# Performance work log

Hardware: AMD Instinct MI355X
Metric: run time of the kernel (lower is better)

Reference implementation:

```python
import jax, jax.numpy as jnp
import numpy as np

N_NODE = 100000
N_EDGE = 500000
IN_DIM = 128
OUT_DIM = 128
ATTN_DIM = 64
N_REL = 200
N_Q = 64


def setup_inputs() -> dict:
    key = jax.random.key(0)
    ks = jax.random.split(key, 24)
    # edge table: columns [r_idx, _, rel, _, tau, sub, obj]
    r_idx = jax.random.randint(ks[0], (N_EDGE,), 0, N_Q, dtype=jnp.int32)
    rel = jax.random.randint(ks[1], (N_EDGE,), 0, 2 * N_REL + 1, dtype=jnp.int32)
    tau = jax.random.randint(ks[2], (N_EDGE,), -1, 366, dtype=jnp.int32)  # -1 -> q_tau fallback
    sub = jax.random.randint(ks[3], (N_EDGE,), 0, N_NODE, dtype=jnp.int32)
    obj = jax.random.randint(ks[4], (N_EDGE,), 0, N_NODE, dtype=jnp.int32)
    zeros = jnp.zeros((N_EDGE,), jnp.int32)
    edges = jnp.stack([r_idx, zeros, rel, zeros, tau, sub, obj], axis=1)

    def lin(k, fan_in, fan_out):
        return jax.random.normal(k, (fan_in, fan_out), jnp.float32) * (1.0 / np.sqrt(fan_in))

    return {
        "q_sub": jax.random.randint(ks[5], (N_Q,), 0, N_NODE, dtype=jnp.int32),
        "q_rel": jax.random.randint(ks[6], (N_Q,), 0, 2 * N_REL + 1, dtype=jnp.int32),
        "q_tau": 180,
        "hidden": jax.random.normal(ks[7], (N_NODE, IN_DIM), jnp.float32),
        "edges": edges,
        "n_node": N_NODE,
        "old_nodes_new_idx": jax.random.randint(ks[8], (1000,), 0, N_NODE, dtype=jnp.int32),
        "rela_embed": jax.random.normal(ks[9], (2 * N_REL + 1, IN_DIM), jnp.float32),
        "Ws_w": lin(ks[10], IN_DIM, ATTN_DIM),
        "Wr_w": lin(ks[11], IN_DIM, ATTN_DIM),
        "Wqr_w": lin(ks[12], IN_DIM, ATTN_DIM),
        "Wqr_b": jnp.zeros((ATTN_DIM,), jnp.float32),
        "Wtau_w": lin(ks[13], IN_DIM, ATTN_DIM),
        "w_alpha_w": lin(ks[14], ATTN_DIM, 1),
        "w_alpha_b": jnp.zeros((1,), jnp.float32),
        "W_h_w": lin(ks[15], IN_DIM, OUT_DIM),
        "W_h_s_w": lin(ks[16], IN_DIM, OUT_DIM),
        "weight_t1": jax.random.normal(ks[17], (1, IN_DIM), jnp.float32),
        "bias_t1": jax.random.normal(ks[18], (1, IN_DIM), jnp.float32),
        "weight_t2": jax.random.normal(ks[19], (1, IN_DIM), jnp.float32),
        "bias_t2": jax.random.normal(ks[20], (1, IN_DIM), jnp.float32),
    }


def reference(q_sub, q_rel, q_tau, hidden, edges, n_node, old_nodes_new_idx,
              rela_embed, Ws_w, Wr_w, Wqr_w, Wqr_b, Wtau_w,
              w_alpha_w, w_alpha_b, W_h_w, W_h_s_w,
              weight_t1, bias_t1, weight_t2, bias_t2):
    sub = edges[:, 5]
    rel = edges[:, 2]
    obj = edges[:, 6]
    tau = edges[:, 4]
    r_idx = edges[:, 0]

    hs = hidden[sub]                       # [E, in_dim] gather
    hr = rela_embed[rel]                   # [E, in_dim]
    h_qr = rela_embed[q_rel][r_idx]        # [E, in_dim]

    tau = jnp.where(tau >= 0, tau, q_tau)
    delta = (tau - q_tau).astype(hidden.dtype)[:, None]  # [E, 1]
    h_tau = weight_t1 * delta + bias_t1 + jnp.sin(weight_t2 * delta + bias_t2)

    message = hs + hr + h_tau              # [E, in_dim]

    attn = jax.nn.relu(hs @ Ws_w + hr @ Wr_w + (h_qr @ Wqr_w + Wqr_b) + h_tau @ Wtau_w)
    alpha = jax.nn.sigmoid(attn @ w_alpha_w + w_alpha_b)  # [E, 1]

    msg = alpha * message
    msg_s = (1.0 - alpha) * message

    agg = jax.ops.segment_sum(msg, obj, num_segments=n_node)      # [n_node, in_dim]
    agg_s = jax.ops.segment_sum(msg_s, obj, num_segments=n_node)

    hidden_new = agg @ W_h_w       # act is identity (default lambda x: x)
    hidden_new_s = agg_s @ W_h_s_w
    return hidden_new, hidden_new_s
```

## Files before the change

### kernel.cpp

```cpp
#include <hip/hip_runtime.h>
#include <math.h>

#define N_NODE   100000
#define N_EDGE   500000
#define IN_DIM   128
#define OUT_DIM  128
#define ATTN_DIM 64
#define N_RELTAB 401
#define N_QRY    64
#define N_TAU    366

#define SCAN_BLK     256
#define N_SCAN_BLKS  ((N_NODE + SCAN_BLK - 1) / SCAN_BLK)

typedef unsigned int  uint;
typedef unsigned short ushort;
typedef __attribute__((ext_vector_type(8))) short bf16x8;
typedef __attribute__((ext_vector_type(4))) float f32x4;

__device__ __forceinline__ float bfl(uint u)  { return __uint_as_float(u << 16); }
__device__ __forceinline__ float bfh(uint u)  { return __uint_as_float(u & 0xFFFF0000u); }
__device__ __forceinline__ uint  f2bfbits(float f) {
    uint u = __float_as_uint(f);
    return (u + 0x7FFFu + ((u >> 16) & 1u)) >> 16;
}
__device__ __forceinline__ uint  pack2(float lo, float hi) {
    return f2bfbits(lo) | (f2bfbits(hi) << 16);
}

__global__ void build_tables(const int* __restrict__ q_rel,
                             const int* __restrict__ q_tau_p,
                             const float* __restrict__ rela_embed,
                             const float* __restrict__ Wr_w,
                             const float* __restrict__ Wqr_w,
                             const float* __restrict__ Wqr_b,
                             const float* __restrict__ Wtau_w,
                             const float* __restrict__ w_t1,
                             const float* __restrict__ b_t1,
                             const float* __restrict__ w_t2,
                             const float* __restrict__ b_t2,
                             const float* __restrict__ W_h_w,
                             const float* __restrict__ W_h_s_w,
                             const float* __restrict__ Ws_w,
                             uint* __restrict__ rel_attn_bf,
                             uint* __restrict__ qr_attn_bf,
                             uint* __restrict__ tau_attn_bf,
                             uint* __restrict__ rel_msg_bf,
                             uint* __restrict__ tau_msg_bf,
                             ushort* __restrict__ wT_bf,
                             ushort* __restrict__ wsT_bf) {
    __shared__ float srow[IN_DIM];
    __shared__ float sattn[ATTN_DIM];
    const int b = blockIdx.x;
    const int t = threadIdx.x;

    if (b < N_TAU) {
        const int q_tau = *q_tau_p;
        const float delta = (float)(b - q_tau);
        float v = w_t1[t] * delta + b_t1[t] + sinf(w_t2[t] * delta + b_t2[t]);
        srow[t] = v;
        __syncthreads();
        if (t < 64) tau_msg_bf[b * 64 + t] = pack2(srow[2 * t], srow[2 * t + 1]);
        if (t < ATTN_DIM) {
            float acc = 0.f;
            #pragma unroll 8
            for (int d = 0; d < IN_DIM; ++d)
                acc += srow[d] * Wtau_w[d * ATTN_DIM + t];
            sattn[t] = acc;
        }
        __syncthreads();
        if (t < 32) tau_attn_bf[b * 32 + t] = pack2(sattn[2 * t], sattn[2 * t + 1]);
    } else if (b < N_TAU + N_RELTAB) {
        const int r = b - N_TAU;
        srow[t] = rela_embed[r * IN_DIM + t];
        __syncthreads();
        if (t < 64) rel_msg_bf[r * 64 + t] = pack2(srow[2 * t], srow[2 * t + 1]);
        if (t < ATTN_DIM) {
            float acc = 0.f;
            #pragma unroll 8
            for (int d = 0; d < IN_DIM; ++d)
                acc += srow[d] * Wr_w[d * ATTN_DIM + t];
            sattn[t] = acc;
        }
        __syncthreads();
        if (t < 32) rel_attn_bf[r * 32 + t] = pack2(sattn[2 * t], sattn[2 * t + 1]);
    } else if (b < N_TAU + N_RELTAB + N_QRY) {
        const int i = b - N_TAU - N_RELTAB;
        const int r = q_rel[i];
        srow[t] = rela_embed[r * IN_DIM + t];
        __syncthreads();
        if (t < ATTN_DIM) {
            float acc = Wqr_b[t];
            #pragma unroll 8
            for (int d = 0; d < IN_DIM; ++d)
                acc += srow[d] * Wqr_w[d * ATTN_DIM + t];
            sattn[t] = acc;
        }
        __syncthreads();
        if (t < 32) qr_attn_bf[i * 32 + t] = pack2(sattn[2 * t], sattn[2 * t + 1]);
    } else {
        const int w = b - (N_TAU + N_RELTAB + N_QRY);
        if (w < 2) {
            const float* Wsrc = w ? W_h_s_w : W_h_w;
            ushort* dst = wT_bf + (size_t)w * 128 * 128;
            for (int k = 0; k < 128; ++k)
                dst[t * 128 + k] = (ushort)f2bfbits(Wsrc[k * 128 + t]);
        } else {
            for (int n = 0; n < 64; ++n)
                wsT_bf[n * 128 + t] = (ushort)f2bfbits(Ws_w[t * ATTN_DIM + n]);
        }
    }
}

__global__ __launch_bounds__(256) void node_attn_mfma(const float* __restrict__ hidden,
                                                      const ushort* __restrict__ wsT_bf,
                                                      uint* __restrict__ hid_bf_u,
                                                      ushort* __restrict__ A_node) {
    const int wave = threadIdx.x >> 6;
    const int lane = threadIdx.x & 63;
    const int m    = lane & 15;
    const int quad = lane >> 4;
    const int row0 = blockIdx.x * 64 + wave * 16;
    const int row  = row0 + m;
    const int rowc = min(row, N_NODE - 1);

    const float* hsrc = hidden + (size_t)rowc * IN_DIM;
    ushort* hdst = (ushort*)hid_bf_u + (size_t)rowc * 128;

    bf16x8 afr[4];
    #pragma unroll
    for (int ks = 0; ks < 4; ++ks) {
        const int k0 = ks * 32 + quad * 8;
        const float4 v0 = *(const float4*)(hsrc + k0);
        const float4 v1 = *(const float4*)(hsrc + k0 + 4);
        union { uint u[4]; bf16x8 v; } cvt;
        cvt.u[0] = pack2(v0.x, v0.y);
        cvt.u[1] = pack2(v0.z, v0.w);
        cvt.u[2] = pack2(v1.x, v1.y);
        cvt.u[3] = pack2(v1.z, v1.w);
        afr[ks] = cvt.v;
        if (row < N_NODE) *(bf16x8*)(hdst + k0) = cvt.v;
    }

    f32x4 acc[4] = {};
    #pragma unroll
    for (int ks = 0; ks < 4; ++ks) {
        #pragma unroll
        for (int ct = 0; ct < 4; ++ct) {
            const bf16x8 wfr = *(const bf16x8*)(wsT_bf + (ct * 16 + m) * 128 + ks * 32 + quad * 8);
            acc[ct] = __builtin_amdgcn_mfma_f32_16x16x32_bf16(wfr, afr[ks], acc[ct], 0, 0, 0);
        }
    }

    if (row < N_NODE) {
        #pragma unroll
        for (int ct = 0; ct < 4; ++ct) {
            uint2 pk;
            pk.x = pack2(acc[ct][0], acc[ct][1]);
            pk.y = pack2(acc[ct][2], acc[ct][3]);
            *(uint2*)(A_node + (size_t)row * 64 + ct * 16 + quad * 4) = pk;
        }
    }
}

__global__ __launch_bounds__(256) void count_edges(const int* __restrict__ edges,
                                                   int* __restrict__ count) {
    const int e = blockIdx.x * 256 + threadIdx.x;
    if (e < N_EDGE) {
        const int obj = edges[(size_t)e * 7 + 6];
        atomicAdd(&count[obj], 1);
    }
}

__global__ __launch_bounds__(SCAN_BLK) void scan_partial(const int* __restrict__ count,
                                                         int* __restrict__ partial) {
    __shared__ int lds[SCAN_BLK];
    const int i = blockIdx.x * SCAN_BLK + threadIdx.x;
    lds[threadIdx.x] = (i < N_NODE) ? count[i] : 0;
    __syncthreads();
    for (int s = SCAN_BLK / 2; s > 0; s >>= 1) {
        if (threadIdx.x < s) lds[threadIdx.x] += lds[threadIdx.x + s];
        __syncthreads();
    }
    if (threadIdx.x == 0) partial[blockIdx.x] = lds[0];
}

__global__ __launch_bounds__(512) void scan_partials(const int* __restrict__ partial,
                                                     int* __restrict__ blk_off) {
    __shared__ int lds[512];
    const int t = threadIdx.x;
    lds[t] = (t < N_SCAN_BLKS) ? partial[t] : 0;
    __syncthreads();
    for (int d = 1; d < 512; d <<= 1) {
        int v = (t >= d) ? lds[t - d] : 0;
        __syncthreads();
        lds[t] += v;
        __syncthreads();
    }
    if (t < N_SCAN_BLKS) blk_off[t] = (t == 0) ? 0 : lds[t - 1];
}

__global__ __launch_bounds__(SCAN_BLK) void scan_apply(const int* __restrict__ count,
                                                       const int* __restrict__ blk_off,
                                                       int* __restrict__ off,
                                                       int* __restrict__ cursor) {
    __shared__ int lds[SCAN_BLK];
    const int t = threadIdx.x;
    const int i = blockIdx.x * SCAN_BLK + t;
    const int v = (i < N_NODE) ? count[i] : 0;
    lds[t] = v;
    __syncthreads();
    for (int d = 1; d < SCAN_BLK; d <<= 1) {
        int x = (t >= d) ? lds[t - d] : 0;
        __syncthreads();
        lds[t] += x;
        __syncthreads();
    }
    const int excl = blk_off[blockIdx.x] + lds[t] - v;
    if (i < N_NODE) { off[i] = excl; cursor[i] = excl; }
    if (i == N_NODE - 1) off[N_NODE] = excl + v;
}

__global__ __launch_bounds__(256) void alpha_fill(const int* __restrict__ edges,
                                                  const int* __restrict__ q_tau_p,
                                                  const uint* __restrict__ A_node_bf,
                                                  const uint* __restrict__ rel_attn_bf,
                                                  const uint* __restrict__ qr_attn_bf,
                                                  const uint* __restrict__ tau_attn_bf,
                                                  const float* __restrict__ w_alpha_w,
                                                  const float* __restrict__ w_alpha_b,
                                                  int* __restrict__ cursor,
                                                  int4* __restrict__ recs) {
    const int t = threadIdx.x;
    const int q = t & 3;
    const int e = blockIdx.x * 64 + (t >> 2);
    if (e >= N_EDGE) return;

    const int* ed = edges + (size_t)e * 7;
    const int r_idx = ed[0];
    const int rel   = ed[2];
    const int tau   = ed[4];
    const int sub   = ed[5];
    const int obj   = ed[6];
    const int q_tau = *q_tau_p;
    const int tidx  = (tau >= 0) ? tau : q_tau;

    const uint4*  pa = (const uint4*)(A_node_bf  + (size_t)sub * 32) + q * 2;
    const uint4*  pr = (const uint4*)(rel_attn_bf + rel   * 32) + q * 2;
    const uint4*  pq = (const uint4*)(qr_attn_bf  + r_idx * 32) + q * 2;
    const uint4*  pt = (const uint4*)(tau_attn_bf + tidx  * 32) + q * 2;
    const float4* wv = (const float4*)w_alpha_w + q * 4;

    float acc = 0.f;

#define DOT_UINT(va, vr, vq, vt, wlo, whi) do {                                  \
        const float x0 = bfl(va) + bfl(vr) + bfl(vq) + bfl(vt);                  \
        const float x1 = bfh(va) + bfh(vr) + bfh(vq) + bfh(vt);                  \
        acc = fmaf(fmaxf(x0, 0.f), (wlo), fmaf(fmaxf(x1, 0.f), (whi), acc));     \
    } while (0)

    #pragma unroll
    for (int c = 0; c < 2; ++c) {
        const uint4  ua = pa[c];
        const uint4  ur = pr[c];
        const uint4  uq = pq[c];
        const uint4  ut = pt[c];
        const float4 w0 = wv[c * 2];
        const float4 w1 = wv[c * 2 + 1];
        DOT_UINT(ua.x, ur.x, uq.x, ut.x, w0.x, w0.y);
        DOT_UINT(ua.y, ur.y, uq.y, ut.y, w0.z, w0.w);
        DOT_UINT(ua.z, ur.z, uq.z, ut.z, w1.x, w1.y);
        DOT_UINT(ua.w, ur.w, uq.w, ut.w, w1.z, w1.w);
    }
#undef DOT_UINT

    acc += __shfl_xor(acc, 1, 64);
    acc += __shfl_xor(acc, 2, 64);

    if (q == 0) {
        const float alpha = 1.f / (1.f + __expf(-(acc + w_alpha_b[0])));
        const int pos = atomicAdd(&cursor[obj], 1);
        recs[pos] = make_int4(sub, rel, tidx, __float_as_int(alpha));
    }
}

__global__ __launch_bounds__(256) void aggregate(const int* __restrict__ off,
                                                 const int4* __restrict__ recs,
                                                 const uint* __restrict__ hid_bf,
                                                 const uint* __restrict__ rel_msg_bf,
                                                 const uint* __restrict__ tau_msg_bf,
                                                 uint* __restrict__ agg_bf) {
    const int wave = threadIdx.x >> 6;
    const int lane = threadIdx.x & 63;
    const int n = blockIdx.x * 4 + wave;
    const int j0 = off[n];
    const int j1 = off[n + 1];

    float t0 = 0.f, t1 = 0.f;
    float a0 = 0.f, a1 = 0.f;
    int j = j0;
    for (; j + 1 < j1; j += 2) {
        const int4 rA = recs[j];
        const int4 rB = recs[j + 1];
        const uint hA = hid_bf[(size_t)rA.x * 64 + lane];
        const uint hB = hid_bf[(size_t)rB.x * 64 + lane];
        const uint eA = rel_msg_bf[rA.y * 64 + lane];
        const uint eB = rel_msg_bf[rB.y * 64 + lane];
        const uint uA = tau_msg_bf[rA.z * 64 + lane];
        const uint uB = tau_msg_bf[rB.z * 64 + lane];
        const float alA = __int_as_float(rA.w);
        const float alB = __int_as_float(rB.w);
        const float m0A = bfl(hA) + bfl(eA) + bfl(uA);
        const float m1A = bfh(hA) + bfh(eA) + bfh(uA);
        const float m0B = bfl(hB) + bfl(eB) + bfl(uB);
        const float m1B = bfh(hB) + bfh(eB) + bfh(uB);
        t0 += m0A + m0B;  t1 += m1A + m1B;
        a0 = fmaf(alA, m0A, fmaf(alB, m0B, a0));
        a1 = fmaf(alA, m1A, fmaf(alB, m1B, a1));
    }
    if (j < j1) {
        const int4 rA = recs[j];
        const uint hA = hid_bf[(size_t)rA.x * 64 + lane];
        const uint eA = rel_msg_bf[rA.y * 64 + lane];
        const uint uA = tau_msg_bf[rA.z * 64 + lane];
        const float alA = __int_as_float(rA.w);
        const float m0A = bfl(hA) + bfl(eA) + bfl(uA);
        const float m1A = bfh(hA) + bfh(eA) + bfh(uA);
        t0 += m0A;  t1 += m1A;
        a0 = fmaf(alA, m0A, a0);
        a1 = fmaf(alA, m1A, a1);
    }
    agg_bf[(size_t)n * 64 + lane] = pack2(a0, a1);
    agg_bf[(size_t)(N_NODE + n) * 64 + lane] = pack2(t0 - a0, t1 - a1);
}

__global__ __launch_bounds__(256) void final_gemm_mfma(const uint* __restrict__ agg_bf,
                                                       const ushort* __restrict__ wT_bf,
                                                       float* __restrict__ out) {
    const int halfsel = blockIdx.y;
    const ushort* W = wT_bf + (size_t)halfsel * 128 * 128;
    const ushort* A = (const ushort*)(agg_bf + (size_t)halfsel * N_NODE * 64);
    float* O = out + (size_t)halfsel * N_NODE * 128;

    const int wave = threadIdx.x >> 6;
    const int lane = threadIdx.x & 63;
    const int m    = lane & 15;
    const int quad = lane >> 4;
    const int row0 = blockIdx.x * 64 + wave * 16;

    const int node = row0 + m;
    const ushort* arow = A + (size_t)min(node, N_NODE - 1) * 128;

    bf16x8 bfrag[4];
    #pragma unroll
    for (int ks = 0; ks < 4; ++ks)
        bfrag[ks] = *(const bf16x8*)(arow + ks * 32 + quad * 8);

    f32x4 acc[8] = {};
    #pragma unroll
    for (int ks = 0; ks < 4; ++ks) {
        #pragma unroll
        for (int ct = 0; ct < 8; ++ct) {
            const bf16x8 wfr = *(const bf16x8*)(W + (ct * 16 + m) * 128 + ks * 32 + quad * 8);
            acc[ct] = __builtin_amdgcn_mfma_f32_16x16x32_bf16(wfr, bfrag[ks], acc[ct], 0, 0, 0);
        }
    }

    if (node < N_NODE) {
        float* orow_p = O + (size_t)node * 128 + quad * 4;
        #pragma unroll
        for (int ct = 0; ct < 8; ++ct)
            *(f32x4*)(orow_p + ct * 16) = acc[ct];
    }
}

extern "C" void kernel_launch(void* const* d_in, const int* in_sizes, int n_in,
                              void* d_out, int out_size, void* d_ws, size_t ws_size,
                              hipStream_t stream) {
    const int*   q_rel      = (const int*)d_in[1];
    const int*   q_tau_p    = (const int*)d_in[2];
    const float* hidden     = (const float*)d_in[3];
    const int*   edges      = (const int*)d_in[4];
    const float* rela_embed = (const float*)d_in[7];
    const float* Ws_w       = (const float*)d_in[8];
    const float* Wr_w       = (const float*)d_in[9];
    const float* Wqr_w      = (const float*)d_in[10];
    const float* Wqr_b      = (const float*)d_in[11];
    const float* Wtau_w     = (const float*)d_in[12];
    const float* w_alpha_w  = (const float*)d_in[13];
    const float* w_alpha_b  = (const float*)d_in[14];
    const float* W_h_w      = (const float*)d_in[15];
    const float* W_h_s_w    = (const float*)d_in[16];
    const float* w_t1       = (const float*)d_in[17];
    const float* b_t1       = (const float*)d_in[18];
    const float* w_t2       = (const float*)d_in[19];
    const float* b_t2       = (const float*)d_in[20];

    char* p = (char*)d_ws;
    uint* hid_bf      = (uint*)p;                 p += (size_t)N_NODE * 64 * 4;
    uint* agg_bf      = (uint*)p;                 p += (size_t)2 * N_NODE * 64 * 4;
    uint* A_node_bf   = (uint*)p;                 p += (size_t)N_NODE * 32 * 4;
    int4* recs        = (int4*)p;                 p += (size_t)N_EDGE * 16;
    uint* rel_attn_bf = (uint*)p;                 p += N_RELTAB * 32 * 4;
    uint* qr_attn_bf  = (uint*)p;                 p += N_QRY * 32 * 4;
    uint* tau_attn_bf = (uint*)p;                 p += N_TAU * 32 * 4;
    uint* rel_msg_bf  = (uint*)p;                 p += N_RELTAB * 64 * 4;
    uint* tau_msg_bf  = (uint*)p;                 p += N_TAU * 64 * 4;
    ushort* wT_bf     = (ushort*)p;               p += (size_t)2 * 128 * 128 * 2;
    ushort* wsT_bf    = (ushort*)p;               p += (size_t)64 * 128 * 2;
    int*  count       = (int*)p;                  p += N_NODE * 4;
    int*  off         = (int*)p;                  p += (N_NODE + 1) * 4;
    int*  cursor      = (int*)p;                  p += N_NODE * 4;
    int*  partial     = (int*)p;                  p += N_SCAN_BLKS * 4;
    int*  blk_off     = (int*)p;                  p += N_SCAN_BLKS * 4;

    hipMemsetAsync(count, 0, (size_t)N_NODE * sizeof(int), stream);

    build_tables<<<dim3(N_TAU + N_RELTAB + N_QRY + 3), dim3(128), 0, stream>>>(
        q_rel, q_tau_p, rela_embed, Wr_w, Wqr_w, Wqr_b, Wtau_w,
        w_t1, b_t1, w_t2, b_t2, W_h_w, W_h_s_w, Ws_w,
        rel_attn_bf, qr_attn_bf, tau_attn_bf, rel_msg_bf, tau_msg_bf, wT_bf, wsT_bf);

    node_attn_mfma<<<dim3((N_NODE + 63) / 64), dim3(256), 0, stream>>>(
        hidden, wsT_bf, hid_bf, (ushort*)A_node_bf);

    count_edges<<<dim3((N_EDGE + 255) / 256), dim3(256), 0, stream>>>(edges, count);

    scan_partial<<<dim3(N_SCAN_BLKS), dim3(SCAN_BLK), 0, stream>>>(count, partial);
    scan_partials<<<dim3(1), dim3(512), 0, stream>>>(partial, blk_off);
    scan_apply<<<dim3(N_SCAN_BLKS), dim3(SCAN_BLK), 0, stream>>>(count, blk_off, off, cursor);

    alpha_fill<<<dim3((N_EDGE + 63) / 64), dim3(256), 0, stream>>>(
        edges, q_tau_p, A_node_bf, rel_attn_bf, qr_attn_bf, tau_attn_bf,
        w_alpha_w, w_alpha_b, cursor, recs);

    aggregate<<<dim3(N_NODE / 4), dim3(256), 0, stream>>>(
        off, recs, hid_bf, rel_msg_bf, tau_msg_bf, agg_bf);

    final_gemm_mfma<<<dim3((N_NODE + 63) / 64, 2), dim3(256), 0, stream>>>(
        agg_bf, wT_bf, (float*)d_out);
}
```

Before: 381.7 us.

## Fuse aggregation with output GEMM via LDS and merge small setup kernels

The segment aggregation now writes each 16-node tile of bf16 sums into swizzled shared memory, and the same block multiplies it by both output weight matrices with MFMA. This removes the global round trip of the aggregated buffer and one launch. Output weights are pre-laid out in per-lane fragment order so each lane loads its fragment directly. Edge counting is folded into the table-build kernel and the per-block scan partials into the node-attention kernel, which cuts launches. The cost is fewer, larger blocks for the aggregation, with a barrier between the gather and GEMM phases.

```diff
diff --git a/kernel.cpp b/kernel.cpp
--- a/kernel.cpp
+++ b/kernel.cpp
@@ -13,6 +13,10 @@
 #define SCAN_BLK     256
 #define N_SCAN_BLKS  ((N_NODE + SCAN_BLK - 1) / SCAN_BLK)
 
+#define NB_TABLES    (N_TAU + N_RELTAB + N_QRY + 3)
+#define NB_COUNT     ((N_EDGE + 255) / 256)
+#define NB_NODE      ((N_NODE + 63) / 64)
+
 typedef unsigned int  uint;
 typedef unsigned short ushort;
 typedef __attribute__((ext_vector_type(8))) short bf16x8;
@@ -28,7 +32,7 @@
     return f2bfbits(lo) | (f2bfbits(hi) << 16);
 }
 
-__global__ void build_tables(const int* __restrict__ q_rel,
+__global__ __launch_bounds__(256) void build_count(const int* __restrict__ q_rel,
                              const int* __restrict__ q_tau_p,
                              const float* __restrict__ rela_embed,
                              const float* __restrict__ Wr_w,
@@ -42,23 +46,35 @@
                              const float* __restrict__ W_h_w,
                              const float* __restrict__ W_h_s_w,
                              const float* __restrict__ Ws_w,
+                             const int* __restrict__ edges,
                              uint* __restrict__ rel_attn_bf,
                              uint* __restrict__ qr_attn_bf,
                              uint* __restrict__ tau_attn_bf,
                              uint* __restrict__ rel_msg_bf,
                              uint* __restrict__ tau_msg_bf,
-                             ushort* __restrict__ wT_bf,
-                             ushort* __restrict__ wsT_bf) {
+                             ushort* __restrict__ wfrag_bf,
+                             ushort* __restrict__ wsT_bf,
+                             int* __restrict__ count) {
     __shared__ float srow[IN_DIM];
     __shared__ float sattn[ATTN_DIM];
     const int b = blockIdx.x;
     const int t = threadIdx.x;
 
+    if (b >= NB_TABLES) {
+        const int e = (b - NB_TABLES) * 256 + t;
+        if (e < N_EDGE) {
+            const int obj = edges[(size_t)e * 7 + 6];
+            atomicAdd(&count[obj], 1);
+        }
+        return;
+    }
+
     if (b < N_TAU) {
-        const int q_tau = *q_tau_p;
-        const float delta = (float)(b - q_tau);
-        float v = w_t1[t] * delta + b_t1[t] + sinf(w_t2[t] * delta + b_t2[t]);
-        srow[t] = v;
+        if (t < 128) {
+            const int q_tau = *q_tau_p;
+            const float delta = (float)(b - q_tau);
+            srow[t] = w_t1[t] * delta + b_t1[t] + sinf(w_t2[t] * delta + b_t2[t]);
+        }
         __syncthreads();
         if (t < 64) tau_msg_bf[b * 64 + t] = pack2(srow[2 * t], srow[2 * t + 1]);
         if (t < ATTN_DIM) {
@@ -72,7 +88,7 @@
         if (t < 32) tau_attn_bf[b * 32 + t] = pack2(sattn[2 * t], sattn[2 * t + 1]);
     } else if (b < N_TAU + N_RELTAB) {
         const int r = b - N_TAU;
-        srow[t] = rela_embed[r * IN_DIM + t];
+        if (t < 128) srow[t] = rela_embed[r * IN_DIM + t];
         __syncthreads();
         if (t < 64) rel_msg_bf[r * 64 + t] = pack2(srow[2 * t], srow[2 * t + 1]);
         if (t < ATTN_DIM) {
@@ -87,7 +103,7 @@
     } else if (b < N_TAU + N_RELTAB + N_QRY) {
         const int i = b - N_TAU - N_RELTAB;
         const int r = q_rel[i];
-        srow[t] = rela_embed[r * IN_DIM + t];
+        if (t < 128) srow[t] = rela_embed[r * IN_DIM + t];
         __syncthreads();
         if (t < ATTN_DIM) {
             float acc = Wqr_b[t];
@@ -102,20 +118,49 @@
         const int w = b - (N_TAU + N_RELTAB + N_QRY);
         if (w < 2) {
             const float* Wsrc = w ? W_h_s_w : W_h_w;
-            ushort* dst = wT_bf + (size_t)w * 128 * 128;
-            for (int k = 0; k < 128; ++k)
-                dst[t * 128 + k] = (ushort)f2bfbits(Wsrc[k * 128 + t]);
+            ushort* dst = wfrag_bf + (size_t)w * 2048 * 8;
+            for (int r = 0; r < 8; ++r) {
+                const int s  = t * 8 + r;
+                const int ct = s >> 8;
+                const int ks = (s >> 6) & 3;
+                const int l  = s & 63;
+                const int lm = l & 15;
+                const int lq = l >> 4;
+                union { ushort us[8]; uint4 v; } tmp;
+                #pragma unroll
+                for (int j = 0; j < 8; ++j)
+                    tmp.us[j] = (ushort)f2bfbits(Wsrc[(ks * 32 + lq * 8 + j) * 128 + ct * 16 + lm]);
+                *(uint4*)(dst + (size_t)s * 8) = tmp.v;
+            }
         } else {
-            for (int n = 0; n < 64; ++n)
-                wsT_bf[n * 128 + t] = (ushort)f2bfbits(Ws_w[t * ATTN_DIM + n]);
-        }
-    }
-}
-
-__global__ __launch_bounds__(256) void node_attn_mfma(const float* __restrict__ hidden,
+            if (t < 128)
+                for (int n = 0; n < 64; ++n)
+                    wsT_bf[n * 128 + t] = (ushort)f2bfbits(Ws_w[t * ATTN_DIM + n]);
+        }
+    }
+}
+
+__global__ __launch_bounds__(256) void node_attn_scan(const float* __restrict__ hidden,
                                                       const ushort* __restrict__ wsT_bf,
                                                       uint* __restrict__ hid_bf_u,
-                                                      ushort* __restrict__ A_node) {
+                                                      ushort* __restrict__ A_node,
+                                                      const int* __restrict__ count,
+                                                      int* __restrict__ partial) {
+    __shared__ int slds[SCAN_BLK];
+
+    if (blockIdx.x >= NB_NODE) {
+        const int blk = blockIdx.x - NB_NODE;
+        const int i = blk * SCAN_BLK + threadIdx.x;
+        slds[threadIdx.x] = (i < N_NODE) ? count[i] : 0;
+        __syncthreads();
+        for (int s = SCAN_BLK / 2; s > 0; s >>= 1) {
+            if (threadIdx.x < s) slds[threadIdx.x] += slds[threadIdx.x + s];
+            __syncthreads();
+        }
+        if (threadIdx.x == 0) partial[blk] = slds[0];
+        return;
+    }
+
     const int wave = threadIdx.x >> 6;
     const int lane = threadIdx.x & 63;
     const int m    = lane & 15;
@@ -161,28 +206,6 @@
             *(uint2*)(A_node + (size_t)row * 64 + ct * 16 + quad * 4) = pk;
         }
     }
-}
-
-__global__ __launch_bounds__(256) void count_edges(const int* __restrict__ edges,
-                                                   int* __restrict__ count) {
-    const int e = blockIdx.x * 256 + threadIdx.x;
-    if (e < N_EDGE) {
-        const int obj = edges[(size_t)e * 7 + 6];
-        atomicAdd(&count[obj], 1);
-    }
-}
-
-__global__ __launch_bounds__(SCAN_BLK) void scan_partial(const int* __restrict__ count,
-                                                         int* __restrict__ partial) {
-    __shared__ int lds[SCAN_BLK];
-    const int i = blockIdx.x * SCAN_BLK + threadIdx.x;
-    lds[threadIdx.x] = (i < N_NODE) ? count[i] : 0;
-    __syncthreads();
-    for (int s = SCAN_BLK / 2; s > 0; s >>= 1) {
-        if (threadIdx.x < s) lds[threadIdx.x] += lds[threadIdx.x + s];
-        __syncthreads();
-    }
-    if (threadIdx.x == 0) partial[blockIdx.x] = lds[0];
 }
 
 __global__ __launch_bounds__(512) void scan_partials(const int* __restrict__ partial,
@@ -284,94 +307,93 @@
     }
 }
 
-__global__ __launch_bounds__(256) void aggregate(const int* __restrict__ off,
-                                                 const int4* __restrict__ recs,
-                                                 const uint* __restrict__ hid_bf,
-                                                 const uint* __restrict__ rel_msg_bf,
-                                                 const uint* __restrict__ tau_msg_bf,
-                                                 uint* __restrict__ agg_bf) {
+__global__ __launch_bounds__(256) void agg_gemm(const int* __restrict__ off,
+                                                const int4* __restrict__ recs,
+                                                const uint* __restrict__ hid_bf,
+                                                const uint* __restrict__ rel_msg_bf,
+                                                const uint* __restrict__ tau_msg_bf,
+                                                const ushort* __restrict__ wfrag,
+                                                float* __restrict__ out) {
+    __shared__ uint lagg[2 * 16 * 64];
+
     const int wave = threadIdx.x >> 6;
     const int lane = threadIdx.x & 63;
-    const int n = blockIdx.x * 4 + wave;
-    const int j0 = off[n];
-    const int j1 = off[n + 1];
-
-    float t0 = 0.f, t1 = 0.f;
-    float a0 = 0.f, a1 = 0.f;
-    int j = j0;
-    for (; j + 1 < j1; j += 2) {
-        const int4 rA = recs[j];
-        const int4 rB = recs[j + 1];
-        const uint hA = hid_bf[(size_t)rA.x * 64 + lane];
-        const uint hB = hid_bf[(size_t)rB.x * 64 + lane];
-        const uint eA = rel_msg_bf[rA.y * 64 + lane];
-        const uint eB = rel_msg_bf[rB.y * 64 + lane];
-        const uint uA = tau_msg_bf[rA.z * 64 + lane];
-        const uint uB = tau_msg_bf[rB.z * 64 + lane];
-        const float alA = __int_as_float(rA.w);
-        const float alB = __int_as_float(rB.w);
-        const float m0A = bfl(hA) + bfl(eA) + bfl(uA);
-        const float m1A = bfh(hA) + bfh(eA) + bfh(uA);
-        const float m0B = bfl(hB) + bfl(eB) + bfl(uB);
-        const float m1B = bfh(hB) + bfh(eB) + bfh(uB);
-        t0 += m0A + m0B;  t1 += m1A + m1B;
-        a0 = fmaf(alA, m0A, fmaf(alB, m0B, a0));
-        a1 = fmaf(alA, m1A, fmaf(alB, m1B, a1));
-    }
-    if (j < j1) {
-        const int4 rA = recs[j];
-        const uint hA = hid_bf[(size_t)rA.x * 64 + lane];
-        const uint eA = rel_msg_bf[rA.y * 64 + lane];
-        const uint uA = tau_msg_bf[rA.z * 64 + lane];
-        const float alA = __int_as_float(rA.w);
-        const float m0A = bfl(hA) + bfl(eA) + bfl(uA);
-        const float m1A = bfh(hA) + bfh(eA) + bfh(uA);
-        t0 += m0A;  t1 += m1A;
-        a0 = fmaf(alA, m0A, a0);
-        a1 = fmaf(alA, m1A, a1);
-    }
-    agg_bf[(size_t)n * 64 + lane] = pack2(a0, a1);
-    agg_bf[(size_t)(N_NODE + n) * 64 + lane] = pack2(t0 - a0, t1 - a1);
-}
-
-__global__ __launch_bounds__(256) void final_gemm_mfma(const uint* __restrict__ agg_bf,
-                                                       const ushort* __restrict__ wT_bf,
-                                                       float* __restrict__ out) {
-    const int halfsel = blockIdx.y;
-    const ushort* W = wT_bf + (size_t)halfsel * 128 * 128;
-    const ushort* A = (const ushort*)(agg_bf + (size_t)halfsel * N_NODE * 64);
-    float* O = out + (size_t)halfsel * N_NODE * 128;
-
-    const int wave = threadIdx.x >> 6;
-    const int lane = threadIdx.x & 63;
+    const int tile = blockIdx.x * 16;
+
+    #pragma unroll
+    for (int k = 0; k < 4; ++k) {
+        const int n16 = wave * 4 + k;
+        const int n = tile + n16;
+        const int j0 = off[n];
+        const int j1 = off[n + 1];
+
+        float t0 = 0.f, t1 = 0.f;
+        float a0 = 0.f, a1 = 0.f;
+        int j = j0;
+        for (; j + 1 < j1; j += 2) {
+            const int4 rA = recs[j];
+            const int4 rB = recs[j + 1];
+            const uint hA = hid_bf[(size_t)rA.x * 64 + lane];
+            const uint hB = hid_bf[(size_t)rB.x * 64 + lane];
+            const uint eA = rel_msg_bf[rA.y * 64 + lane];
+            const uint eB = rel_msg_bf[rB.y * 64 + lane];
+            const uint uA = tau_msg_bf[rA.z * 64 + lane];
+            const uint uB = tau_msg_bf[rB.z * 64 + lane];
+            const float alA = __int_as_float(rA.w);
+            const float alB = __int_as_float(rB.w);
+            const float m0A = bfl(hA) + bfl(eA) + bfl(uA);
+            const float m1A = bfh(hA) + bfh(eA) + bfh(uA);
+            const float m0B = bfl(hB) + bfl(eB) + bfl(uB);
+            const float m1B = bfh(hB) + bfh(eB) + bfh(uB);
+            t0 += m0A + m0B;  t1 += m1A + m1B;
+            a0 = fmaf(alA, m0A, fmaf(alB, m0B, a0));
+            a1 = fmaf(alA, m1A, fmaf(alB, m1B, a1));
+        }
+        if (j < j1) {
+            const int4 rA = recs[j];
+            const uint hA = hid_bf[(size_t)rA.x * 64 + lane];
+            const uint eA = rel_msg_bf[rA.y * 64 + lane];
+            const uint uA = tau_msg_bf[rA.z * 64 + lane];
+            const float alA = __int_as_float(rA.w);
+            const float m0A = bfl(hA) + bfl(eA) + bfl(uA);
+            const float m1A = bfh(hA) + bfh(eA) + bfh(uA);
+            t0 += m0A;  t1 += m1A;
+            a0 = fmaf(alA, m0A, a0);
+            a1 = fmaf(alA, m1A, a1);
+        }
+        const int gw = (((lane >> 2) ^ (n16 & 7)) << 2) | (lane & 3);
+        lagg[n16 * 64 + gw]        = pack2(a0, a1);
+        lagg[1024 + n16 * 64 + gw] = pack2(t0 - a0, t1 - a1);
+    }
+    __syncthreads();
+
+    const int half = wave & 1;
+    const int ctg  = (wave >> 1) * 4;
     const int m    = lane & 15;
     const int quad = lane >> 4;
-    const int row0 = blockIdx.x * 64 + wave * 16;
-
-    const int node = row0 + m;
-    const ushort* arow = A + (size_t)min(node, N_NODE - 1) * 128;
 
     bf16x8 bfrag[4];
     #pragma unroll
-    for (int ks = 0; ks < 4; ++ks)
-        bfrag[ks] = *(const bf16x8*)(arow + ks * 32 + quad * 8);
-
-    f32x4 acc[8] = {};
+    for (int ks = 0; ks < 4; ++ks) {
+        const int g = (ks * 4 + quad) ^ (m & 7);
+        bfrag[ks] = *(const bf16x8*)&lagg[half * 1024 + m * 64 + g * 4];
+    }
+
+    f32x4 acc[4] = {};
     #pragma unroll
     for (int ks = 0; ks < 4; ++ks) {
         #pragma unroll
-        for (int ct = 0; ct < 8; ++ct) {
-            const bf16x8 wfr = *(const bf16x8*)(W + (ct * 16 + m) * 128 + ks * 32 + quad * 8);
-            acc[ct] = __builtin_amdgcn_mfma_f32_16x16x32_bf16(wfr, bfrag[ks], acc[ct], 0, 0, 0);
-        }
-    }
-
-    if (node < N_NODE) {
-        float* orow_p = O + (size_t)node * 128 + quad * 4;
-        #pragma unroll
-        for (int ct = 0; ct < 8; ++ct)
-            *(f32x4*)(orow_p + ct * 16) = acc[ct];
-    }
+        for (int c = 0; c < 4; ++c) {
+            const bf16x8 wfr = *(const bf16x8*)(wfrag +
+                ((size_t)(((half * 8 + ctg + c) * 4 + ks) * 64 + lane)) * 8);
+            acc[c] = __builtin_amdgcn_mfma_f32_16x16x32_bf16(wfr, bfrag[ks], acc[c], 0, 0, 0);
+        }
+    }
+
+    float* O = out + (size_t)half * N_NODE * 128 + (size_t)(tile + m) * 128;
+    #pragma unroll
+    for (int c = 0; c < 4; ++c)
+        *(f32x4*)(O + (ctg + c) * 16 + quad * 4) = acc[c];
 }
 
 extern "C" void kernel_launch(void* const* d_in, const int* in_sizes, int n_in,
@@ -398,7 +420,6 @@
 
     char* p = (char*)d_ws;
     uint* hid_bf      = (uint*)p;                 p += (size_t)N_NODE * 64 * 4;
-    uint* agg_bf      = (uint*)p;                 p += (size_t)2 * N_NODE * 64 * 4;
     uint* A_node_bf   = (uint*)p;                 p += (size_t)N_NODE * 32 * 4;
     int4* recs        = (int4*)p;                 p += (size_t)N_EDGE * 16;
     uint* rel_attn_bf = (uint*)p;                 p += N_RELTAB * 32 * 4;
@@ -406,7 +427,7 @@
     uint* tau_attn_bf = (uint*)p;                 p += N_TAU * 32 * 4;
     uint* rel_msg_bf  = (uint*)p;                 p += N_RELTAB * 64 * 4;
     uint* tau_msg_bf  = (uint*)p;                 p += N_TAU * 64 * 4;
-    ushort* wT_bf     = (ushort*)p;               p += (size_t)2 * 128 * 128 * 2;
+    ushort* wfrag_bf  = (ushort*)p;               p += (size_t)2 * 2048 * 8 * 2;
     ushort* wsT_bf    = (ushort*)p;               p += (size_t)64 * 128 * 2;
     int*  count       = (int*)p;                  p += N_NODE * 4;
     int*  off         = (int*)p;                  p += (N_NODE + 1) * 4;
@@ -416,17 +437,15 @@
 
     hipMemsetAsync(count, 0, (size_t)N_NODE * sizeof(int), stream);
 
-    build_tables<<<dim3(N_TAU + N_RELTAB + N_QRY + 3), dim3(128), 0, stream>>>(
+    build_count<<<dim3(NB_TABLES + NB_COUNT), dim3(256), 0, stream>>>(
         q_rel, q_tau_p, rela_embed, Wr_w, Wqr_w, Wqr_b, Wtau_w,
-        w_t1, b_t1, w_t2, b_t2, W_h_w, W_h_s_w, Ws_w,
-        rel_attn_bf, qr_attn_bf, tau_attn_bf, rel_msg_bf, tau_msg_bf, wT_bf, wsT_bf);
-
-    node_attn_mfma<<<dim3((N_NODE + 63) / 64), dim3(256), 0, stream>>>(
-        hidden, wsT_bf, hid_bf, (ushort*)A_node_bf);
-
-    count_edges<<<dim3((N_EDGE + 255) / 256), dim3(256), 0, stream>>>(edges, count);
-
-    scan_partial<<<dim3(N_SCAN_BLKS), dim3(SCAN_BLK), 0, stream>>>(count, partial);
+        w_t1, b_t1, w_t2, b_t2, W_h_w, W_h_s_w, Ws_w, edges,
+        rel_attn_bf, qr_attn_bf, tau_attn_bf, rel_msg_bf, tau_msg_bf,
+        wfrag_bf, wsT_bf, count);
+
+    node_attn_scan<<<dim3(NB_NODE + N_SCAN_BLKS), dim3(256), 0, stream>>>(
+        hidden, wsT_bf, hid_bf, (ushort*)A_node_bf, count, partial);
+
     scan_partials<<<dim3(1), dim3(512), 0, stream>>>(partial, blk_off);
     scan_apply<<<dim3(N_SCAN_BLKS), dim3(SCAN_BLK), 0, stream>>>(count, blk_off, off, cursor);
 
@@ -434,9 +453,6 @@
         edges, q_tau_p, A_node_bf, rel_attn_bf, qr_attn_bf, tau_attn_bf,
         w_alpha_w, w_alpha_b, cursor, recs);
 
-    aggregate<<<dim3(N_NODE / 4), dim3(256), 0, stream>>>(
-        off, recs, hid_bf, rel_msg_bf, tau_msg_bf, agg_bf);
-
-    final_gemm_mfma<<<dim3((N_NODE + 63) / 64, 2), dim3(256), 0, stream>>>(
-        agg_bf, wT_bf, (float*)d_out);
-}
+    agg_gemm<<<dim3(N_NODE / 16), dim3(256), 0, stream>>>(
+        off, recs, hid_bf, rel_msg_bf, tau_msg_bf, wfrag_bf, (float*)d_out);
+}
```

New measurement: 322.8 us. 15.4% less time.
